# Performance work log

Measured on AMD Instinct MI355X. Metric: run time of the kernel, lower is better.

Reference implementation:

```python
import jax, jax.numpy as jnp
import numpy as np

T = 4096
H = 1024
K = 32  # type_size; embedding table has K+1 rows


def setup_inputs() -> dict:
    key = jax.random.key(0)
    k1, k2, k3, k4 = jax.random.split(key, 4)
    event = jax.random.randint(k1, (T,), 0, K)
    duration = jax.random.uniform(k2, (T,), dtype=jnp.float32)
    w_r = jax.random.normal(k3, (2 * H, 7 * H), dtype=jnp.float32) * (1.0 / np.sqrt(2 * H))
    b_r = jnp.zeros((7 * H,), dtype=jnp.float32)
    emb_event = jax.random.normal(k4, (K + 1, H), dtype=jnp.float32)
    return {"event": event, "duration": duration, "w_r": w_r, "b_r": b_r, "emb_event": emb_event}


def reference(event, duration, w_r, b_r, emb_event):
    h = w_r.shape[0] // 2
    emb = emb_event[event]  # [T, H] gather of per-event embeddings

    def step(carry, inp):
        h_d, c, c_bar = carry
        e_t, d_t = inp
        feed = jnp.concatenate([e_t, h_d])              # [2H]
        gates = feed @ w_r + b_r                        # [7H]
        g_i, g_f, g_z, g_o, g_ib, g_fb, g_dl = jnp.split(gates, 7)
        g_i = jax.nn.sigmoid(g_i)
        g_f = jax.nn.sigmoid(g_f)
        g_z = jnp.tanh(g_z)
        g_o = jax.nn.sigmoid(g_o)
        g_ib = jax.nn.sigmoid(g_ib)
        g_fb = jax.nn.sigmoid(g_fb)
        g_dl = jax.nn.softplus(g_dl)
        c_t = g_f * c + g_i * g_z
        c_bar_t = g_fb * c_bar + g_ib * g_z
        h_t = g_o * jnp.tanh(c_t)
        # continuous-time decay toward c_bar over duration d_t
        c_d = c_bar_t + (c_t - c_bar_t) * jnp.exp(-g_dl * d_t)
        h_d_t = g_o * jnp.tanh(c_d)
        return (h_d_t, c_t, c_bar_t), (h_t, c_t, c_bar_t, g_o, g_dl)

    z = jnp.zeros((h,), dtype=w_r.dtype)
    init = (z, z, z)
    _, (h_seq, c_seq, c_bar_seq, o_seq, delta_seq) = jax.lax.scan(step, init, (emb, duration))
    return jnp.stack((h_seq, c_seq, c_bar_seq, o_seq, delta_seq))  # [5, T, H]
```

## Files before the change

kernel.cpp:

```cpp
#include <hip/hip_runtime.h>
#include <math.h>

#define TT 4096
#define HH 1024
#define GC 7168
#define KK 33
#define NB 256
#define NT 448

__device__ float g_P[KK * GC];
__device__ unsigned long long g_hd64[2 * HH];

__global__ __launch_bounds__(256) void setup_kernel(const float* __restrict__ w_r,
                                                    const float* __restrict__ b_r,
                                                    const float* __restrict__ emb) {
  const int j = blockIdx.x * 256 + threadIdx.x;
  if (j < 2 * HH) g_hd64[j] = 0ULL;
  float acc[KK];
  const float bj = b_r[j];
#pragma unroll
  for (int k = 0; k < KK; ++k) acc[k] = bj;
  for (int i = 0; i < HH; ++i) {
    const float w = w_r[(size_t)i * GC + j];
#pragma unroll
    for (int k = 0; k < KK; ++k) acc[k] = fmaf(emb[k * HH + i], w, acc[k]);
  }
#pragma unroll
  for (int k = 0; k < KK; ++k) g_P[k * GC + j] = acc[k];
}

__global__ __launch_bounds__(NT) void ctlstm_kernel(const int* __restrict__ event,
                                                    const float* __restrict__ duration,
                                                    const float* __restrict__ w_r,
                                                    float* __restrict__ out) {
  __shared__ __align__(16) float hd_lds[HH];
  __shared__ float gred[7][4];
  const int tid = threadIdx.x;
  const int b = blockIdx.x;
  const int g = tid >> 6;
  const int l = tid & 63;
  const int jj = l & 3;
  const int r = l >> 2;
  const int col = g * HH + 4 * b + jj;

  float4 w4[16];
#pragma unroll
  for (int k = 0; k < 16; ++k) {
    const float* wp = w_r + (size_t)(HH + 4 * r + 64 * k) * GC + col;
    w4[k].x = wp[0];
    w4[k].y = wp[GC];
    w4[k].z = wp[2 * (size_t)GC];
    w4[k].w = wp[3 * (size_t)GC];
  }
  for (int i = tid; i < HH; i += NT) hd_lds[i] = 0.f;
  float c_st = 0.f, cb_st = 0.f;
  __syncthreads();

  for (int t = 0; t < TT; ++t) {
    float pval = 0.f;
    if (l < 4) pval = g_P[event[t] * GC + col];

    float acc = 0.f;
#pragma unroll
    for (int k = 0; k < 16; ++k) {
      const float4 h4 = *(const float4*)&hd_lds[4 * r + 64 * k];
      acc = fmaf(w4[k].x, h4.x, acc);
      acc = fmaf(w4[k].y, h4.y, acc);
      acc = fmaf(w4[k].z, h4.z, acc);
      acc = fmaf(w4[k].w, h4.w, acc);
    }
    acc += __shfl_xor(acc, 4);
    acc += __shfl_xor(acc, 8);
    acc += __shfl_xor(acc, 16);
    acc += __shfl_xor(acc, 32);
    if (l < 4) {
      float v = acc + pval;
      if (g == 2) v = tanhf(v);
      else if (g == 6) v = fmaxf(v, 0.f) + log1pf(expf(-fabsf(v)));
      else v = 1.f / (1.f + expf(-v));
      gred[g][jj] = v;
    }
    __syncthreads();

    if (tid < 4) {
      const float si = gred[0][tid], sf = gred[1][tid], tz = gred[2][tid];
      const float so = gred[3][tid], sib = gred[4][tid], sfb = gred[5][tid];
      const float sp = gred[6][tid];
      const float c_n = fmaf(sf, c_st, si * tz);
      const float cb_n = fmaf(sfb, cb_st, sib * tz);
      c_st = c_n;
      cb_st = cb_n;
      const float dt = duration[t];
      const float cd = fmaf(c_n - cb_n, expf(-sp * dt), cb_n);
      const int j = 4 * b + tid;
      if (t < TT - 1) {
        const float hdv = so * tanhf(cd);
        const unsigned long long pk =
            ((unsigned long long)(unsigned)(t + 1) << 32) | (unsigned long long)__float_as_uint(hdv);
        (void)__hip_atomic_exchange(&g_hd64[((t + 1) & 1) * HH + j], pk,
                                    __ATOMIC_RELAXED, __HIP_MEMORY_SCOPE_AGENT);
      }
      const size_t o = (size_t)t * HH + j;
      out[o] = so * tanhf(c_n);
      out[(size_t)TT * HH + o] = c_n;
      out[2 * (size_t)TT * HH + o] = cb_n;
      out[3 * (size_t)TT * HH + o] = so;
      out[4 * (size_t)TT * HH + o] = sp;
    }

    if (t < TT - 1 && tid < 256) {
      const unsigned int want = (unsigned)(t + 1);
      const unsigned long long* buf = &g_hd64[((t + 1) & 1) * HH];
      bool d0 = false, d1 = false, d2 = false, d3 = false;
      for (;;) {
        if (!d0) {
          const unsigned long long p =
              __hip_atomic_load(&buf[tid], __ATOMIC_RELAXED, __HIP_MEMORY_SCOPE_AGENT);
          if ((unsigned)(p >> 32) == want) { hd_lds[tid] = __uint_as_float((unsigned)p); d0 = true; }
        }
        if (!d1) {
          const unsigned long long p =
              __hip_atomic_load(&buf[tid + 256], __ATOMIC_RELAXED, __HIP_MEMORY_SCOPE_AGENT);
          if ((unsigned)(p >> 32) == want) { hd_lds[tid + 256] = __uint_as_float((unsigned)p); d1 = true; }
        }
        if (!d2) {
          const unsigned long long p =
              __hip_atomic_load(&buf[tid + 512], __ATOMIC_RELAXED, __HIP_MEMORY_SCOPE_AGENT);
          if ((unsigned)(p >> 32) == want) { hd_lds[tid + 512] = __uint_as_float((unsigned)p); d2 = true; }
        }
        if (!d3) {
          const unsigned long long p =
              __hip_atomic_load(&buf[tid + 768], __ATOMIC_RELAXED, __HIP_MEMORY_SCOPE_AGENT);
          if ((unsigned)(p >> 32) == want) { hd_lds[tid + 768] = __uint_as_float((unsigned)p); d3 = true; }
        }
        if (d0 && d1 && d2 && d3) break;
        __builtin_amdgcn_s_sleep(1);
      }
    }
    __syncthreads();
  }
}

extern "C" void kernel_launch(void* const* d_in, const int* in_sizes, int n_in,
                              void* d_out, int out_size, void* d_ws, size_t ws_size,
                              hipStream_t stream) {
  const int* event = (const int*)d_in[0];
  const float* duration = (const float*)d_in[1];
  const float* w_r = (const float*)d_in[2];
  const float* b_r = (const float*)d_in[3];
  const float* emb = (const float*)d_in[4];
  float* out = (float*)d_out;
  setup_kernel<<<GC / 256, 256, 0, stream>>>(w_r, b_r, emb);
  ctlstm_kernel<<<NB, NT, 0, stream>>>(event, duration, w_r, out);
}
```

Baseline: 13.92 ms.

## Prefetch next-step inputs, self-write own h slice, and tighten spin polling

```diff
diff --git a/kernel.cpp b/kernel.cpp
--- a/kernel.cpp
+++ b/kernel.cpp
@@ -54,11 +54,21 @@
   }
   for (int i = tid; i < HH; i += NT) hd_lds[i] = 0.f;
   float c_st = 0.f, cb_st = 0.f;
+
+  const bool is_poller = (tid >= 64 && tid < 320);
+  const int p = tid - 64;
+  unsigned self_mask = 0u;
+  if (is_poller && ((p >> 2) == (b & 63))) self_mask = 1u << (b >> 6);
+
+  float pval = 0.f;
+  if (l < 4) pval = g_P[event[0] * GC + col];
+  float du = 0.f;
+  if (tid < 4) du = duration[0];
   __syncthreads();
 
   for (int t = 0; t < TT; ++t) {
-    float pval = 0.f;
-    if (l < 4) pval = g_P[event[t] * GC + col];
+    const bool not_last = (t < TT - 1);
+    const int ev_next = not_last ? event[t + 1] : 0;
 
     float acc = 0.f;
 #pragma unroll
@@ -82,6 +92,8 @@
     }
     __syncthreads();
 
+    if (not_last && l < 4) pval = g_P[ev_next * GC + col];
+
     if (tid < 4) {
       const float si = gred[0][tid], sf = gred[1][tid], tz = gred[2][tid];
       const float so = gred[3][tid], sib = gred[4][tid], sfb = gred[5][tid];
@@ -90,15 +102,16 @@
       const float cb_n = fmaf(sfb, cb_st, sib * tz);
       c_st = c_n;
       cb_st = cb_n;
-      const float dt = duration[t];
-      const float cd = fmaf(c_n - cb_n, expf(-sp * dt), cb_n);
+      const float cd = fmaf(c_n - cb_n, expf(-sp * du), cb_n);
       const int j = 4 * b + tid;
-      if (t < TT - 1) {
+      if (not_last) {
         const float hdv = so * tanhf(cd);
         const unsigned long long pk =
             ((unsigned long long)(unsigned)(t + 1) << 32) | (unsigned long long)__float_as_uint(hdv);
         (void)__hip_atomic_exchange(&g_hd64[((t + 1) & 1) * HH + j], pk,
                                     __ATOMIC_RELAXED, __HIP_MEMORY_SCOPE_AGENT);
+        hd_lds[j] = hdv;
+        du = duration[t + 1];
       }
       const size_t o = (size_t)t * HH + j;
       out[o] = so * tanhf(c_n);
@@ -108,34 +121,20 @@
       out[4 * (size_t)TT * HH + o] = sp;
     }
 
-    if (t < TT - 1 && tid < 256) {
-      const unsigned int want = (unsigned)(t + 1);
+    if (not_last && is_poller) {
+      const unsigned want = (unsigned)(t + 1);
       const unsigned long long* buf = &g_hd64[((t + 1) & 1) * HH];
-      bool d0 = false, d1 = false, d2 = false, d3 = false;
-      for (;;) {
-        if (!d0) {
-          const unsigned long long p =
-              __hip_atomic_load(&buf[tid], __ATOMIC_RELAXED, __HIP_MEMORY_SCOPE_AGENT);
-          if ((unsigned)(p >> 32) == want) { hd_lds[tid] = __uint_as_float((unsigned)p); d0 = true; }
-        }
-        if (!d1) {
-          const unsigned long long p =
-              __hip_atomic_load(&buf[tid + 256], __ATOMIC_RELAXED, __HIP_MEMORY_SCOPE_AGENT);
-          if ((unsigned)(p >> 32) == want) { hd_lds[tid + 256] = __uint_as_float((unsigned)p); d1 = true; }
-        }
-        if (!d2) {
-          const unsigned long long p =
-              __hip_atomic_load(&buf[tid + 512], __ATOMIC_RELAXED, __HIP_MEMORY_SCOPE_AGENT);
-          if ((unsigned)(p >> 32) == want) { hd_lds[tid + 512] = __uint_as_float((unsigned)p); d2 = true; }
-        }
-        if (!d3) {
-          const unsigned long long p =
-              __hip_atomic_load(&buf[tid + 768], __ATOMIC_RELAXED, __HIP_MEMORY_SCOPE_AGENT);
-          if ((unsigned)(p >> 32) == want) { hd_lds[tid + 768] = __uint_as_float((unsigned)p); d3 = true; }
-        }
-        if (d0 && d1 && d2 && d3) break;
-        __builtin_amdgcn_s_sleep(1);
-      }
+      unsigned done = self_mask;
+      do {
+        const unsigned long long v0 = __hip_atomic_load(&buf[p],       __ATOMIC_RELAXED, __HIP_MEMORY_SCOPE_AGENT);
+        const unsigned long long v1 = __hip_atomic_load(&buf[p + 256], __ATOMIC_RELAXED, __HIP_MEMORY_SCOPE_AGENT);
+        const unsigned long long v2 = __hip_atomic_load(&buf[p + 512], __ATOMIC_RELAXED, __HIP_MEMORY_SCOPE_AGENT);
+        const unsigned long long v3 = __hip_atomic_load(&buf[p + 768], __ATOMIC_RELAXED, __HIP_MEMORY_SCOPE_AGENT);
+        if (!(done & 1u) && (unsigned)(v0 >> 32) == want) { hd_lds[p]       = __uint_as_float((unsigned)v0); done |= 1u; }
+        if (!(done & 2u) && (unsigned)(v1 >> 32) == want) { hd_lds[p + 256] = __uint_as_float((unsigned)v1); done |= 2u; }
+        if (!(done & 4u) && (unsigned)(v2 >> 32) == want) { hd_lds[p + 512] = __uint_as_float((unsigned)v2); done |= 4u; }
+        if (!(done & 8u) && (unsigned)(v3 >> 32) == want) { hd_lds[p + 768] = __uint_as_float((unsigned)v3); done |= 8u; }
+      } while (done != 15u);
     }
     __syncthreads();
   }
```

Result: slower. 16.37 ms (+17.6%).
